# Performance work log

Hardware: AMD Instinct MI355X
Metric: run time of the kernel (lower is better)

Reference implementation:

```python
import jax, jax.numpy as jnp
import numpy as np

EMBED_DIM = 768
NUM_HEADS = 8
HEAD_DIM = EMBED_DIM // NUM_HEADS  # 96
SCALE = HEAD_DIM ** -0.5


def setup_inputs() -> dict:
    key = jax.random.key(0)
    k1, k2, k3 = jax.random.split(key, 3)
    x = jax.random.normal(k1, (2, 4096, EMBED_DIM), dtype=jnp.float32)
    # nn.Linear weights stored [out, in]; init scaled like kaiming-uniform-ish
    w_qkv = jax.random.normal(k2, (3 * EMBED_DIM, EMBED_DIM), dtype=jnp.float32) * (EMBED_DIM ** -0.5)
    w_proj = jax.random.normal(k3, (EMBED_DIM, EMBED_DIM), dtype=jnp.float32) * (EMBED_DIM ** -0.5)
    return {"x": x, "w_qkv": w_qkv, "w_proj": w_proj}


def reference(x, w_qkv, w_proj):
    B, N, C = x.shape
    H, D = NUM_HEADS, C // NUM_HEADS
    qkv = jnp.einsum('bnc,oc->bno', x, w_qkv)          # [B,N,3C]
    qkv = qkv.reshape(B, N, 3, H, D).transpose(2, 0, 3, 1, 4)  # [3,B,H,N,D]
    q, k, v = qkv[0], qkv[1], qkv[2]
    attn = jnp.einsum('bhnd,bhmd->bhnm', q, k) * SCALE  # [B,H,N,N]
    attn = jax.nn.softmax(attn, axis=-1)
    out = jnp.einsum('bhnm,bhmd->bhnd', attn, v)        # [B,H,N,D]
    out = out.transpose(0, 2, 1, 3).reshape(B, N, C)
    out = jnp.einsum('bnc,oc->bno', out, w_proj)        # proj (no bias)
    return out  # dropout p=0.0 -> identity
```

## Files before the change

kernel.cpp:

```cpp
#include <hip/hip_runtime.h>

typedef __bf16 bf16;
typedef __attribute__((ext_vector_type(8))) __bf16 bf16x8;
typedef __attribute__((ext_vector_type(2))) __bf16 bf16x2;
typedef __attribute__((ext_vector_type(4))) float f32x4;
typedef __attribute__((ext_vector_type(16))) float f32x16;
typedef __attribute__((ext_vector_type(8))) unsigned short ushort8;
typedef __attribute__((ext_vector_type(4))) unsigned short ushort4v;

__device__ __forceinline__ unsigned short f2bf(float f) {
    union { float f; unsigned int u; } v; v.f = f;
    unsigned int u = v.u;
    return (unsigned short)((u + 0x7fffu + ((u >> 16) & 1u)) >> 16);
}

#if __has_builtin(__builtin_amdgcn_cvt_pk_bf16_f32)
__device__ __forceinline__ unsigned int pk2bf(float a, float b) {
    union { bf16x2 v; unsigned int u; } c;
    c.v = __builtin_amdgcn_cvt_pk_bf16_f32(a, b);
    return c.u;
}
#else
__device__ __forceinline__ unsigned int pk2bf(float a, float b) {
    return (unsigned int)f2bf(a) | ((unsigned int)f2bf(b) << 16);
}
#endif

__device__ __forceinline__ f32x4 mfma16(bf16x8 a, bf16x8 b, f32x4 c) {
    return __builtin_amdgcn_mfma_f32_16x16x32_bf16(a, b, c, 0, 0, 0);
}
__device__ __forceinline__ f32x16 mfma32(bf16x8 a, bf16x8 b, f32x16 c) {
    return __builtin_amdgcn_mfma_f32_32x32x16_bf16(a, b, c, 0, 0, 0);
}

__global__ void cvt3_f32_bf16(const float* __restrict__ x, const float* __restrict__ wq,
                              const float* __restrict__ wp,
                              unsigned short* __restrict__ xb, unsigned short* __restrict__ wqb,
                              unsigned short* __restrict__ wpb) {
    int i = blockIdx.x * 256 + threadIdx.x;
    const float* in; unsigned short* out; int base;
    if (i < 1572864)      { in = x;  out = xb;  base = i; }
    else if (i < 2015232) { in = wq; out = wqb; base = i - 1572864; }
    else if (i < 2162688) { in = wp; out = wpb; base = i - 2015232; }
    else return;
    float4 f = reinterpret_cast<const float4*>(in)[base];
    union { ushort4v v; unsigned int u[2]; } o;
    o.u[0] = pk2bf(f.x, f.y);
    o.u[1] = pk2bf(f.z, f.w);
    reinterpret_cast<ushort4v*>(out)[base] = o.v;
}

__device__ __forceinline__ int kperm(int k5) {
    return (k5 & 3) | (((k5 >> 3) & 1) << 2) | (((k5 >> 4) & 1) << 3) | (((k5 >> 2) & 1) << 4);
}

__global__ __launch_bounds__(256) void qkv_gemm(const unsigned short* __restrict__ A,
                                                const unsigned short* __restrict__ W,
                                                unsigned short* __restrict__ Qf,
                                                unsigned short* __restrict__ Kf,
                                                unsigned short* __restrict__ Vf) {
    __shared__ __align__(16) unsigned short As[128 * 40];
    __shared__ __align__(16) unsigned short Bs[128 * 40];
    const int t = threadIdx.x;
    const int w = t >> 6, l = t & 63;
    const int wm = (w >> 1) * 64, wn = (w & 1) * 64;
    const int lr = l & 15, lq = l >> 4;
    const int m0 = blockIdx.y * 128, n0 = blockIdx.x * 128;
    f32x4 acc[4][4] = {};
    for (int k0 = 0; k0 < 768; k0 += 32) {
        __syncthreads();
#pragma unroll
        for (int i = 0; i < 2; ++i) {
            int v = t + i * 256;
            int r = v >> 2, c8 = (v & 3) * 8;
            *reinterpret_cast<ushort8*>(&As[r * 40 + c8]) =
                *reinterpret_cast<const ushort8*>(&A[(m0 + r) * 768 + k0 + c8]);
            *reinterpret_cast<ushort8*>(&Bs[r * 40 + c8]) =
                *reinterpret_cast<const ushort8*>(&W[(n0 + r) * 768 + k0 + c8]);
        }
        __syncthreads();
        bf16x8 af[4], bfr[4];
#pragma unroll
        for (int mt = 0; mt < 4; ++mt)
            af[mt] = *reinterpret_cast<const bf16x8*>(&As[(wm + mt * 16 + lr) * 40 + lq * 8]);
#pragma unroll
        for (int nt = 0; nt < 4; ++nt)
            bfr[nt] = *reinterpret_cast<const bf16x8*>(&Bs[(wn + nt * 16 + lr) * 40 + lq * 8]);
#pragma unroll
        for (int mt = 0; mt < 4; ++mt)
#pragma unroll
            for (int nt = 0; nt < 4; ++nt)
                acc[mt][nt] = mfma16(af[mt], bfr[nt], acc[mt][nt]);
    }
#pragma unroll
    for (int nt = 0; nt < 4; ++nt) {
        int gn = n0 + wn + nt * 16 + lr;
        int tsel = gn / 768, rem = gn - tsel * 768;
        int hh8 = rem / 96, d = rem - hh8 * 96;
#pragma unroll
        for (int mt = 0; mt < 4; ++mt) {
#pragma unroll
            for (int r = 0; r < 4; ++r) {
                int gm = m0 + wm + mt * 16 + lq * 4 + r;
                int b = gm >> 12, n = gm & 4095;
                int bh = b * 8 + hh8;
                float val = acc[mt][nt][r];
                if (tsel == 0) {
                    int qg = n >> 5, l31 = n & 31;
                    int kq = d >> 4, h2 = (d >> 3) & 1, j = d & 7;
                    Qf[((((bh * 128 + qg) * 6 + kq)) << 9) + ((h2 * 32 + l31) << 3) + j] =
                        f2bf(val * 0.14724444f);
                } else if (tsel == 1) {
                    int kg = n >> 5, p5 = kperm(n & 31);
                    int kq = d >> 4, h2 = (d >> 3) & 1, j = d & 7;
                    Kf[((((bh * 128 + kg) * 6 + kq)) << 9) + ((h2 * 32 + p5) << 3) + j] =
                        f2bf(val);
                } else {
                    int kg = n >> 5, r5 = n & 31;
                    int f = r5 >> 4, hv = (r5 >> 3) & 1, j = r5 & 7;
                    int dn = d >> 5, dl = d & 31;
                    Vf[((((bh * 128 + kg) * 6 + dn * 2 + f)) << 9) + ((hv * 32 + dl) << 3) + j] =
                        f2bf(val);
                }
            }
        }
    }
}

__global__ __launch_bounds__(256, 2) void attn_kernel(const unsigned short* __restrict__ Qf,
                                                      const unsigned short* __restrict__ Kf,
                                                      const unsigned short* __restrict__ Vf,
                                                      unsigned short* __restrict__ Og) {
    __shared__ __align__(16) float red[4608];
    const int t = threadIdx.x;
    const int w = t >> 6, l = t & 63;
    const int wr = w >> 1, wk = w & 1;
    const int l31 = l & 31, h = l >> 5;
    const int b0 = blockIdx.x;
    const int kk = b0 >> 3;
    const int bh = (b0 & 7) * 2 + (kk >> 5);
    const int q0 = (kk & 31) * 128;
    const int voff = l << 3;

    bf16x8 aq[2][6];
#pragma unroll
    for (int qn = 0; qn < 2; ++qn) {
        long qb = ((long)((bh * 128 + (q0 >> 5) + wr * 2 + qn) * 6)) << 9;
#pragma unroll
        for (int kq = 0; kq < 6; ++kq)
            aq[qn][kq] = *reinterpret_cast<const bf16x8*>(&Qf[qb + (kq << 9) + voff]);
    }

    bf16x8 ones8;
#pragma unroll
    for (int i = 0; i < 8; ++i) ones8[i] = (__bf16)1.0f;

    f32x16 acc[2][3] = {};
    f32x16 acc_l[2] = {};

    for (int it = 0; it < 64; ++it) {
        const int kt = wk * 64 + it;
        const long kbase = ((long)((bh * 128 + kt) * 6)) << 9;
        f32x16 s[2] = {};
#pragma unroll
        for (int kq = 0; kq < 6; ++kq) {
            bf16x8 bk = *reinterpret_cast<const bf16x8*>(&Kf[kbase + (kq << 9) + voff]);
            s[0] = mfma32(bk, aq[0][kq], s[0]);
            s[1] = mfma32(bk, aq[1][kq], s[1]);
        }
        union PF { unsigned int u[4]; bf16x8 v8; } p[2][2];
#pragma unroll
        for (int qn = 0; qn < 2; ++qn) {
            float e[16];
#pragma unroll
            for (int r = 0; r < 16; ++r) e[r] = __builtin_amdgcn_exp2f(s[qn][r]);
#pragma unroll
            for (int f = 0; f < 2; ++f) {
                p[qn][f].u[0] = pk2bf(e[4 * f + 0], e[4 * f + 1]);
                p[qn][f].u[1] = pk2bf(e[4 * f + 2], e[4 * f + 3]);
                p[qn][f].u[2] = pk2bf(e[8 + 4 * f + 0], e[8 + 4 * f + 1]);
                p[qn][f].u[3] = pk2bf(e[8 + 4 * f + 2], e[8 + 4 * f + 3]);
            }
        }
#pragma unroll
        for (int dn = 0; dn < 3; ++dn) {
#pragma unroll
            for (int f = 0; f < 2; ++f) {
                bf16x8 vb = *reinterpret_cast<const bf16x8*>(
                    &Vf[kbase + ((dn * 2 + f) << 9) + voff]);
                acc[0][dn] = mfma32(p[0][f].v8, vb, acc[0][dn]);
                acc[1][dn] = mfma32(p[1][f].v8, vb, acc[1][dn]);
            }
        }
#pragma unroll
        for (int qn = 0; qn < 2; ++qn)
#pragma unroll
            for (int f = 0; f < 2; ++f)
                acc_l[qn] = mfma32(p[qn][f].v8, ones8, acc_l[qn]);
    }

    const int rbase = (wr * 64 + l) * 36;
#pragma unroll
    for (int ps = 0; ps < 3; ++ps) {
        __syncthreads();
        if (wk == 1) {
#pragma unroll
            for (int c = 0; c < 2; ++c) {
                int c2 = ps * 2 + c, qn = c2 / 3, dn = c2 % 3;
#pragma unroll
                for (int u = 0; u < 4; ++u) {
                    f32x4 tmp;
#pragma unroll
                    for (int j = 0; j < 4; ++j) tmp[j] = acc[qn][dn][u * 4 + j];
                    *reinterpret_cast<f32x4*>(&red[rbase + c * 16 + u * 4]) = tmp;
                }
            }
        }
        __syncthreads();
        if (wk == 0) {
#pragma unroll
            for (int c = 0; c < 2; ++c) {
                int c2 = ps * 2 + c, qn = c2 / 3, dn = c2 % 3;
#pragma unroll
                for (int u = 0; u < 4; ++u) {
                    f32x4 tmp = *reinterpret_cast<const f32x4*>(&red[rbase + c * 16 + u * 4]);
#pragma unroll
                    for (int j = 0; j < 4; ++j) acc[qn][dn][u * 4 + j] += tmp[j];
                }
            }
        }
    }
    __syncthreads();
    if (wk == 1) {
#pragma unroll
        for (int qn = 0; qn < 2; ++qn)
#pragma unroll
            for (int u = 0; u < 4; ++u) {
                f32x4 tmp;
#pragma unroll
                for (int j = 0; j < 4; ++j) tmp[j] = acc_l[qn][u * 4 + j];
                *reinterpret_cast<f32x4*>(&red[rbase + qn * 16 + u * 4]) = tmp;
            }
    }
    __syncthreads();
    if (wk == 0) {
#pragma unroll
        for (int qn = 0; qn < 2; ++qn)
#pragma unroll
            for (int u = 0; u < 4; ++u) {
                f32x4 tmp = *reinterpret_cast<const f32x4*>(&red[rbase + qn * 16 + u * 4]);
#pragma unroll
                for (int j = 0; j < 4; ++j) acc_l[qn][u * 4 + j] += tmp[j];
            }
        const int b = bh >> 3, head = bh & 7;
#pragma unroll
        for (int qn = 0; qn < 2; ++qn) {
#pragma unroll
            for (int reg = 0; reg < 16; ++reg) {
                int qloc = (reg & 3) + 8 * (reg >> 2) + 4 * h;
                int n = q0 + wr * 64 + qn * 32 + qloc;
                float inv = 1.f / acc_l[qn][reg];
                int rowoff = (b * 4096 + n) * 768 + head * 96;
#pragma unroll
                for (int dn = 0; dn < 3; ++dn)
                    Og[rowoff + dn * 32 + l31] = f2bf(acc[qn][dn][reg] * inv);
            }
        }
    }
}

__global__ __launch_bounds__(256) void proj_gemm(const unsigned short* __restrict__ A,
                                                 const unsigned short* __restrict__ W,
                                                 float* __restrict__ out) {
    __shared__ __align__(16) unsigned short As[128 * 40];
    __shared__ __align__(16) unsigned short Bs[128 * 40];
    const int t = threadIdx.x;
    const int w = t >> 6, l = t & 63;
    const int wm = (w >> 1) * 64, wn = (w & 1) * 64;
    const int lr = l & 15, lq = l >> 4;
    const int m0 = blockIdx.y * 128, n0 = blockIdx.x * 128;
    f32x4 acc[4][4] = {};
    for (int k0 = 0; k0 < 768; k0 += 32) {
        __syncthreads();
#pragma unroll
        for (int i = 0; i < 2; ++i) {
            int v = t + i * 256;
            int r = v >> 2, c8 = (v & 3) * 8;
            *reinterpret_cast<ushort8*>(&As[r * 40 + c8]) =
                *reinterpret_cast<const ushort8*>(&A[(m0 + r) * 768 + k0 + c8]);
            *reinterpret_cast<ushort8*>(&Bs[r * 40 + c8]) =
                *reinterpret_cast<const ushort8*>(&W[(n0 + r) * 768 + k0 + c8]);
        }
        __syncthreads();
        bf16x8 af[4], bfr[4];
#pragma unroll
        for (int mt = 0; mt < 4; ++mt)
            af[mt] = *reinterpret_cast<const bf16x8*>(&As[(wm + mt * 16 + lr) * 40 + lq * 8]);
#pragma unroll
        for (int nt = 0; nt < 4; ++nt)
            bfr[nt] = *reinterpret_cast<const bf16x8*>(&Bs[(wn + nt * 16 + lr) * 40 + lq * 8]);
#pragma unroll
        for (int mt = 0; mt < 4; ++mt)
#pragma unroll
            for (int nt = 0; nt < 4; ++nt)
                acc[mt][nt] = mfma16(af[mt], bfr[nt], acc[mt][nt]);
    }
#pragma unroll
    for (int nt = 0; nt < 4; ++nt) {
        int gn = n0 + wn + nt * 16 + lr;
#pragma unroll
        for (int mt = 0; mt < 4; ++mt) {
#pragma unroll
            for (int r = 0; r < 4; ++r) {
                int gm = m0 + wm + mt * 16 + lq * 4 + r;
                out[gm * 768 + gn] = acc[mt][nt][r];
            }
        }
    }
}

extern "C" void kernel_launch(void* const* d_in, const int* in_sizes, int n_in,
                              void* d_out, int out_size, void* d_ws, size_t ws_size,
                              hipStream_t stream) {
    const float* x     = (const float*)d_in[0];
    const float* wqkv  = (const float*)d_in[1];
    const float* wproj = (const float*)d_in[2];
    float* out = (float*)d_out;
    char* ws = (char*)d_ws;
    unsigned short* xb     = (unsigned short*)(ws);
    unsigned short* wqkvb  = (unsigned short*)(ws + 12582912);
    unsigned short* wprojb = (unsigned short*)(ws + 16121856);
    unsigned short* Qf     = (unsigned short*)(ws + 17301504);
    unsigned short* Kf     = (unsigned short*)(ws + 29884416);
    unsigned short* Vf     = (unsigned short*)(ws + 42467328);
    unsigned short* attnb  = xb;

    cvt3_f32_bf16<<<8448, 256, 0, stream>>>(x, wqkv, wproj, xb, wqkvb, wprojb);
    qkv_gemm<<<dim3(18, 64), 256, 0, stream>>>(xb, wqkvb, Qf, Kf, Vf);
    attn_kernel<<<512, 256, 0, stream>>>(Qf, Kf, Vf, attnb);
    proj_gemm<<<dim3(6, 64), 256, 0, stream>>>(attnb, wprojb, out);
}
```

Before: 300.6 us.

## Stage QKV epilogue through LDS and split attention keys across four waves

```diff
diff --git a/kernel.cpp b/kernel.cpp
--- a/kernel.cpp
+++ b/kernel.cpp
@@ -53,14 +53,19 @@
 __device__ __forceinline__ int kperm(int k5) {
     return (k5 & 3) | (((k5 >> 3) & 1) << 2) | (((k5 >> 4) & 1) << 3) | (((k5 >> 2) & 1) << 4);
 }
+__device__ __forceinline__ int kperm_inv(int p5) {
+    return (p5 & 3) | (((p5 >> 4) & 1) << 2) | (((p5 >> 2) & 1) << 3) | (((p5 >> 3) & 1) << 4);
+}
 
 __global__ __launch_bounds__(256) void qkv_gemm(const unsigned short* __restrict__ A,
                                                 const unsigned short* __restrict__ W,
                                                 unsigned short* __restrict__ Qf,
                                                 unsigned short* __restrict__ Kf,
                                                 unsigned short* __restrict__ Vf) {
-    __shared__ __align__(16) unsigned short As[128 * 40];
-    __shared__ __align__(16) unsigned short Bs[128 * 40];
+    __shared__ __align__(16) char smem[40960];
+    unsigned short* As = (unsigned short*)smem;
+    unsigned short* Bs = (unsigned short*)(smem + 20480);
+    unsigned short* T  = (unsigned short*)smem;
     const int t = threadIdx.x;
     const int w = t >> 6, l = t & 63;
     const int wm = (w >> 1) * 64, wn = (w & 1) * 64;
@@ -92,60 +97,97 @@
             for (int nt = 0; nt < 4; ++nt)
                 acc[mt][nt] = mfma16(af[mt], bfr[nt], acc[mt][nt]);
     }
-#pragma unroll
-    for (int nt = 0; nt < 4; ++nt) {
-        int gn = n0 + wn + nt * 16 + lr;
-        int tsel = gn / 768, rem = gn - tsel * 768;
-        int hh8 = rem / 96, d = rem - hh8 * 96;
-#pragma unroll
-        for (int mt = 0; mt < 4; ++mt) {
-#pragma unroll
-            for (int r = 0; r < 4; ++r) {
-                int gm = m0 + wm + mt * 16 + lq * 4 + r;
-                int b = gm >> 12, n = gm & 4095;
-                int bh = b * 8 + hh8;
-                float val = acc[mt][nt][r];
-                if (tsel == 0) {
-                    int qg = n >> 5, l31 = n & 31;
-                    int kq = d >> 4, h2 = (d >> 3) & 1, j = d & 7;
-                    Qf[((((bh * 128 + qg) * 6 + kq)) << 9) + ((h2 * 32 + l31) << 3) + j] =
-                        f2bf(val * 0.14724444f);
-                } else if (tsel == 1) {
-                    int kg = n >> 5, p5 = kperm(n & 31);
-                    int kq = d >> 4, h2 = (d >> 3) & 1, j = d & 7;
-                    Kf[((((bh * 128 + kg) * 6 + kq)) << 9) + ((h2 * 32 + p5) << 3) + j] =
-                        f2bf(val);
-                } else {
-                    int kg = n >> 5, r5 = n & 31;
-                    int f = r5 >> 4, hv = (r5 >> 3) & 1, j = r5 & 7;
-                    int dn = d >> 5, dl = d & 31;
-                    Vf[((((bh * 128 + kg) * 6 + dn * 2 + f)) << 9) + ((hv * 32 + dl) << 3) + j] =
-                        f2bf(val);
-                }
-            }
-        }
-    }
-}
-
-__global__ __launch_bounds__(256, 2) void attn_kernel(const unsigned short* __restrict__ Qf,
+    const int tsel = n0 / 768;
+    __syncthreads();
+    if (tsel < 2) {
+#pragma unroll
+        for (int nt = 0; nt < 4; ++nt)
+#pragma unroll
+            for (int mt = 0; mt < 4; ++mt)
+#pragma unroll
+                for (int r = 0; r < 4; ++r) {
+                    int row = wm + mt * 16 + lq * 4 + r;
+                    int col = wn + nt * 16 + lr;
+                    float val = acc[mt][nt][r];
+                    if (tsel == 0) val *= 0.14724444f;
+                    T[row * 136 + col] = f2bf(val);
+                }
+    } else {
+#pragma unroll
+        for (int nt = 0; nt < 4; ++nt)
+#pragma unroll
+            for (int mt = 0; mt < 4; ++mt)
+#pragma unroll
+                for (int r = 0; r < 4; ++r) {
+                    int row = wm + mt * 16 + lq * 4 + r;
+                    int col = wn + nt * 16 + lr;
+                    T[col * 136 + row] = f2bf(acc[mt][nt][r]);
+                }
+    }
+    __syncthreads();
+    if (tsel < 2) {
+#pragma unroll
+        for (int i = 0; i < 8; ++i) {
+            int idx = t + i * 256;
+            int pos31 = idx & 31;
+            int rest = idx >> 5;
+            int c8 = rest & 15, qg = rest >> 4;
+            int l31 = (tsel == 1) ? kperm_inv(pos31) : pos31;
+            int gncol = n0 + c8 * 8;
+            int rem = gncol - tsel * 768;
+            int head = rem / 96, d = rem - head * 96;
+            int kq = d >> 4, h2 = (d >> 3) & 1;
+            int gm = m0 + qg * 32 + l31;
+            int b = gm >> 12, nn = gm & 4095;
+            int bh = b * 8 + head;
+            long chunk = (long)(bh * 128 + (nn >> 5)) * 6 + kq;
+            ushort8 v8 = *reinterpret_cast<const ushort8*>(&T[(qg * 32 + l31) * 136 + c8 * 8]);
+            unsigned short* dst = (tsel == 0) ? Qf : Kf;
+            *reinterpret_cast<ushort8*>(&dst[(chunk << 9) + ((h2 * 32 + pos31) << 3)]) = v8;
+        }
+    } else {
+#pragma unroll
+        for (int i = 0; i < 8; ++i) {
+            int idx = t + i * 256;
+            int dl = idx & 31;
+            int rr = idx >> 5;
+            int r8 = rr & 15, cmb = rr >> 4;
+            int col = cmb * 32 + dl;
+            int gncol = n0 + col;
+            int rem = gncol - 1536;
+            int head = rem / 96, d = rem - head * 96;
+            int dn = d >> 5;
+            int keybase = m0 + r8 * 8;
+            int b = keybase >> 12, nn = keybase & 4095;
+            int kg = nn >> 5, f = (nn >> 4) & 1, hv = (nn >> 3) & 1;
+            int bh = b * 8 + head;
+            long chunk = (long)(bh * 128 + kg) * 6 + dn * 2 + f;
+            ushort8 v8 = *reinterpret_cast<const ushort8*>(&T[col * 136 + r8 * 8]);
+            *reinterpret_cast<ushort8*>(&Vf[(chunk << 9) + ((hv * 32 + dl) << 3)]) = v8;
+        }
+    }
+}
+
+__global__ __launch_bounds__(256, 4) void attn_kernel(const unsigned short* __restrict__ Qf,
                                                       const unsigned short* __restrict__ Kf,
                                                       const unsigned short* __restrict__ Vf,
                                                       unsigned short* __restrict__ Og) {
-    __shared__ __align__(16) float red[4608];
+    __shared__ __align__(16) float red[64 * 132];
     const int t = threadIdx.x;
     const int w = t >> 6, l = t & 63;
-    const int wr = w >> 1, wk = w & 1;
+    const int wk = w;
     const int l31 = l & 31, h = l >> 5;
     const int b0 = blockIdx.x;
     const int kk = b0 >> 3;
-    const int bh = (b0 & 7) * 2 + (kk >> 5);
-    const int q0 = (kk & 31) * 128;
+    const int bh = (b0 & 7) * 2 + (kk >> 6);
+    const int qt = kk & 63;
+    const int q0 = qt * 64;
     const int voff = l << 3;
 
     bf16x8 aq[2][6];
 #pragma unroll
     for (int qn = 0; qn < 2; ++qn) {
-        long qb = ((long)((bh * 128 + (q0 >> 5) + wr * 2 + qn) * 6)) << 9;
+        long qb = ((long)((bh * 128 + qt * 2 + qn) * 6)) << 9;
 #pragma unroll
         for (int kq = 0; kq < 6; ++kq)
             aq[qn][kq] = *reinterpret_cast<const bf16x8*>(&Qf[qb + (kq << 9) + voff]);
@@ -158,8 +200,8 @@
     f32x16 acc[2][3] = {};
     f32x16 acc_l[2] = {};
 
-    for (int it = 0; it < 64; ++it) {
-        const int kt = wk * 64 + it;
+    for (int it = 0; it < 32; ++it) {
+        const int kt = wk * 32 + it;
         const long kbase = ((long)((bh * 128 + kt) * 6)) << 9;
         f32x16 s[2] = {};
 #pragma unroll
@@ -199,66 +241,63 @@
                 acc_l[qn] = mfma32(p[qn][f].v8, ones8, acc_l[qn]);
     }
 
-    const int rbase = (wr * 64 + l) * 36;
-#pragma unroll
-    for (int ps = 0; ps < 3; ++ps) {
-        __syncthreads();
-        if (wk == 1) {
-#pragma unroll
-            for (int c = 0; c < 2; ++c) {
-                int c2 = ps * 2 + c, qn = c2 / 3, dn = c2 % 3;
+#pragma unroll
+    for (int pwave = 1; pwave < 4; ++pwave) {
+        __syncthreads();
+        if (w == pwave) {
+#pragma unroll
+            for (int qn = 0; qn < 2; ++qn) {
+#pragma unroll
+                for (int dn = 0; dn < 3; ++dn) {
+                    int slot = qn * 3 + dn;
+#pragma unroll
+                    for (int u = 0; u < 4; ++u) {
+                        f32x4 tmp;
+#pragma unroll
+                        for (int j = 0; j < 4; ++j) tmp[j] = acc[qn][dn][u * 4 + j];
+                        *reinterpret_cast<f32x4*>(&red[l * 132 + slot * 16 + u * 4]) = tmp;
+                    }
+                }
 #pragma unroll
                 for (int u = 0; u < 4; ++u) {
                     f32x4 tmp;
 #pragma unroll
-                    for (int j = 0; j < 4; ++j) tmp[j] = acc[qn][dn][u * 4 + j];
-                    *reinterpret_cast<f32x4*>(&red[rbase + c * 16 + u * 4]) = tmp;
-                }
-            }
-        }
-        __syncthreads();
-        if (wk == 0) {
-#pragma unroll
-            for (int c = 0; c < 2; ++c) {
-                int c2 = ps * 2 + c, qn = c2 / 3, dn = c2 % 3;
+                    for (int j = 0; j < 4; ++j) tmp[j] = acc_l[qn][u * 4 + j];
+                    *reinterpret_cast<f32x4*>(&red[l * 132 + (6 + qn) * 16 + u * 4]) = tmp;
+                }
+            }
+        }
+        __syncthreads();
+        if (w == 0) {
+#pragma unroll
+            for (int qn = 0; qn < 2; ++qn) {
+#pragma unroll
+                for (int dn = 0; dn < 3; ++dn) {
+                    int slot = qn * 3 + dn;
+#pragma unroll
+                    for (int u = 0; u < 4; ++u) {
+                        f32x4 tmp = *reinterpret_cast<const f32x4*>(&red[l * 132 + slot * 16 + u * 4]);
+#pragma unroll
+                        for (int j = 0; j < 4; ++j) acc[qn][dn][u * 4 + j] += tmp[j];
+                    }
+                }
 #pragma unroll
                 for (int u = 0; u < 4; ++u) {
-                    f32x4 tmp = *reinterpret_cast<const f32x4*>(&red[rbase + c * 16 + u * 4]);
-#pragma unroll
-                    for (int j = 0; j < 4; ++j) acc[qn][dn][u * 4 + j] += tmp[j];
-                }
-            }
-        }
-    }
-    __syncthreads();
-    if (wk == 1) {
-#pragma unroll
-        for (int qn = 0; qn < 2; ++qn)
-#pragma unroll
-            for (int u = 0; u < 4; ++u) {
-                f32x4 tmp;
-#pragma unroll
-                for (int j = 0; j < 4; ++j) tmp[j] = acc_l[qn][u * 4 + j];
-                *reinterpret_cast<f32x4*>(&red[rbase + qn * 16 + u * 4]) = tmp;
-            }
-    }
-    __syncthreads();
-    if (wk == 0) {
-#pragma unroll
-        for (int qn = 0; qn < 2; ++qn)
-#pragma unroll
-            for (int u = 0; u < 4; ++u) {
-                f32x4 tmp = *reinterpret_cast<const f32x4*>(&red[rbase + qn * 16 + u * 4]);
-#pragma unroll
-                for (int j = 0; j < 4; ++j) acc_l[qn][u * 4 + j] += tmp[j];
-            }
+                    f32x4 tmp = *reinterpret_cast<const f32x4*>(&red[l * 132 + (6 + qn) * 16 + u * 4]);
+#pragma unroll
+                    for (int j = 0; j < 4; ++j) acc_l[qn][u * 4 + j] += tmp[j];
+                }
+            }
+        }
+    }
+    if (w == 0) {
         const int b = bh >> 3, head = bh & 7;
 #pragma unroll
         for (int qn = 0; qn < 2; ++qn) {
 #pragma unroll
             for (int reg = 0; reg < 16; ++reg) {
                 int qloc = (reg & 3) + 8 * (reg >> 2) + 4 * h;
-                int n = q0 + wr * 64 + qn * 32 + qloc;
+                int n = q0 + qn * 32 + qloc;
                 float inv = 1.f / acc_l[qn][reg];
                 int rowoff = (b * 4096 + n) * 768 + head * 96;
 #pragma unroll
@@ -337,6 +376,6 @@
 
     cvt3_f32_bf16<<<8448, 256, 0, stream>>>(x, wqkv, wproj, xb, wqkvb, wprojb);
     qkv_gemm<<<dim3(18, 64), 256, 0, stream>>>(xb, wqkvb, Qf, Kf, Vf);
-    attn_kernel<<<512, 256, 0, stream>>>(Qf, Kf, Vf, attnb);
+    attn_kernel<<<1024, 256, 0, stream>>>(Qf, Kf, Vf, attnb);
     proj_gemm<<<dim3(6, 64), 256, 0, stream>>>(attnb, wprojb, out);
 }
```

Measured after the change: 1.119 ms. +272.3%, slower.
